# Optimization experiments

Hardware: AMD Instinct MI355X
Metric: run time of the kernel (lower is better)

Reference implementation:

```python
import jax, jax.numpy as jnp
import numpy as np

HEADS = 8
DIM_HEAD = 64
SCALE = DIM_HEAD ** -0.5


def setup_inputs() -> dict:
    key = jax.random.key(0)
    k1, k2, k3, k4 = jax.random.split(key, 4)
    dim = 512
    inner = HEADS * DIM_HEAD  # 512
    x = jax.random.normal(k1, (4, 2048, dim), dtype=jnp.float32)
    # torch nn.Linear weight layout: [out_features, in_features]
    w_qkv = jax.random.normal(k2, (inner * 3, dim), dtype=jnp.float32) * (dim ** -0.5)
    w_out = jax.random.normal(k3, (dim, inner), dtype=jnp.float32) * (inner ** -0.5)
    b_out = jax.random.normal(k4, (dim,), dtype=jnp.float32) * 0.01
    return {"x": x, "w_qkv": w_qkv, "w_out": w_out, "b_out": b_out}


def reference(x, w_qkv, w_out, b_out):
    b, n, _ = x.shape
    qkv = x @ w_qkv.T                                   # [b, n, 3*inner]
    q, k, v = jnp.split(qkv, 3, axis=-1)
    def to_heads(t):
        return t.reshape(b, n, HEADS, DIM_HEAD).transpose(0, 2, 1, 3)  # b h n d
    q, k, v = to_heads(q), to_heads(k), to_heads(v)
    dots = jnp.einsum('bhid,bhjd->bhij', q, k) * SCALE  # [b, h, n, n]
    attn = jax.nn.softmax(dots, axis=-1)
    out = jnp.einsum('bhij,bhjd->bhid', attn, v)        # [b, h, n, d]
    out = out.transpose(0, 2, 1, 3).reshape(b, n, HEADS * DIM_HEAD)
    return out @ w_out.T + b_out                        # [b, n, dim]
```

## Files before the change

kernel.cpp:

```cpp
#include <hip/hip_runtime.h>

typedef unsigned int u32;
typedef unsigned short u16;
typedef float f32x4 __attribute__((ext_vector_type(4)));
typedef u32 u32x4 __attribute__((ext_vector_type(4)));
typedef u32 u32x2 __attribute__((ext_vector_type(2)));

__device__ __forceinline__ u16 f2bf(float f) {
    u32 u = __builtin_bit_cast(u32, f);
    u = (u + 0x7FFFu + ((u >> 16) & 1u)) >> 16;
    return (u16)u;
}

__device__ __forceinline__ void mfma16(f32x4& d, const u32x4& a, const u32x4& b) {
    asm("v_mfma_f32_16x16x32_bf16 %0, %1, %2, %0" : "+v"(d) : "v"(a), "v"(b));
}

__device__ __forceinline__ float exp2a(float x) {
    float r;
    asm("v_exp_f32 %0, %1\n\ts_nop 1" : "=v"(r) : "v"(x));
    return r;
}
__device__ __forceinline__ u32 cvtpk(float lo, float hi) {
    u32 r;
    asm("v_cvt_pk_bf16_f32 %0, %1, %2" : "=v"(r) : "v"(lo), "v"(hi));
    return r;
}

__global__ __launch_bounds__(256) void cast_kernel(const float* __restrict__ in,
                                                   u16* __restrict__ out, int n) {
    int i = (blockIdx.x * 256 + threadIdx.x) * 8;
    if (i >= n) return;
    float4 a = *(const float4*)(in + i);
    float4 b = *(const float4*)(in + i + 4);
    u32x4 r;
    r.x = (u32)f2bf(a.x) | ((u32)f2bf(a.y) << 16);
    r.y = (u32)f2bf(a.z) | ((u32)f2bf(a.w) << 16);
    r.z = (u32)f2bf(b.x) | ((u32)f2bf(b.y) << 16);
    r.w = (u32)f2bf(b.z) | ((u32)f2bf(b.w) << 16);
    *(u32x4*)(out + i) = r;
}

template <int MODE>
__global__ __launch_bounds__(256) void gemm_bt(
    const u16* __restrict__ A, const u16* __restrict__ B, int K, int N,
    u16* __restrict__ qo, u16* __restrict__ ko, u16* __restrict__ vto,
    float* __restrict__ fo, const float* __restrict__ bias)
{
    __shared__ __align__(16) u16 Al[128][72];
    __shared__ __align__(16) u16 Bl[128][72];
    const int t = threadIdx.x;
    const int w = t >> 6, l = t & 63;
    const int wr = w >> 1, wc = w & 1;
    const int g = l >> 4, li = l & 15;
    const int m0 = blockIdx.x * 128, n0 = blockIdx.y * 128;

    const f32x4 z = {0.f, 0.f, 0.f, 0.f};
    f32x4 acc[4][4];
#pragma unroll
    for (int mi = 0; mi < 4; ++mi)
#pragma unroll
        for (int ni = 0; ni < 4; ++ni) acc[mi][ni] = z;

    const int srow = t >> 3, sch = (t & 7) * 8;
    for (int k0 = 0; k0 < K; k0 += 64) {
        __syncthreads();
#pragma unroll
        for (int rnd = 0; rnd < 4; ++rnd) {
            int row = srow + rnd * 32;
            u32x4 av = *(const u32x4*)(A + (size_t)(m0 + row) * K + k0 + sch);
            u32x4 bv = *(const u32x4*)(B + (size_t)(n0 + row) * K + k0 + sch);
            *(u32x4*)&Al[row][sch] = av;
            *(u32x4*)&Bl[row][sch] = bv;
        }
        __syncthreads();
#pragma unroll
        for (int ks = 0; ks < 2; ++ks) {
            u32x4 af[4], bf[4];
#pragma unroll
            for (int mi = 0; mi < 4; ++mi)
                af[mi] = *(const u32x4*)&Al[wr * 64 + mi * 16 + li][ks * 32 + g * 8];
#pragma unroll
            for (int ni = 0; ni < 4; ++ni)
                bf[ni] = *(const u32x4*)&Bl[wc * 64 + ni * 16 + li][ks * 32 + g * 8];
#pragma unroll
            for (int mi = 0; mi < 4; ++mi)
#pragma unroll
                for (int ni = 0; ni < 4; ++ni) mfma16(acc[mi][ni], af[mi], bf[ni]);
        }
    }

#pragma unroll
    for (int mi = 0; mi < 4; ++mi) {
#pragma unroll
        for (int ni = 0; ni < 4; ++ni) {
            int o = n0 + wc * 64 + ni * 16 + li;
            int m_base = m0 + wr * 64 + mi * 16 + g * 4;
            if (MODE == 0) {
                int part = o >> 9, oi = o & 511;
                int h = oi >> 6, d = oi & 63;
                int bb = m_base >> 11, nn = m_base & 2047;
                if (part == 2) {
                    u32x2 pv;
                    pv.x = (u32)f2bf(acc[mi][ni][0]) | ((u32)f2bf(acc[mi][ni][1]) << 16);
                    pv.y = (u32)f2bf(acc[mi][ni][2]) | ((u32)f2bf(acc[mi][ni][3]) << 16);
                    *(u32x2*)(vto + ((size_t)(bb * 8 + h) * 64 + d) * 2048 + nn) = pv;
                } else {
                    u16* dst = (part == 0) ? qo : ko;
#pragma unroll
                    for (int r = 0; r < 4; ++r)
                        dst[((size_t)(bb * 8 + h) * 2048 + nn + r) * 64 + d] =
                            f2bf(acc[mi][ni][r]);
                }
            } else {
#pragma unroll
                for (int r = 0; r < 4; ++r)
                    fo[(size_t)(m_base + r) * N + o] = acc[mi][ni][r] + bias[o];
            }
        }
    }
}

__global__ __launch_bounds__(256) void attn_kernel(
    const u16* __restrict__ Q, const u16* __restrict__ Kg,
    const u16* __restrict__ VT, u16* __restrict__ O)
{
    __shared__ __align__(16) u16 Kl[64 * 64];
    __shared__ __align__(16) u16 Vl[64 * 64];
    const int t = threadIdx.x;
    const int w = t >> 6, l = t & 63;
    const int g = l >> 4, li = l & 15;
    const int pair = blockIdx.y;
    const int q0 = blockIdx.x * 128 + w * 32;
    const float CEXP = 0.18033688011112042f;

    u32x4 qf[2][2];
#pragma unroll
    for (int qb = 0; qb < 2; ++qb)
#pragma unroll
        for (int f = 0; f < 2; ++f)
            qf[qb][f] = *(const u32x4*)(Q + ((size_t)pair * 2048 + q0 + qb * 16 + li) * 64
                                          + f * 32 + g * 8);

    const f32x4 z = {0.f, 0.f, 0.f, 0.f};
    f32x4 oacc[2][4];
#pragma unroll
    for (int qb = 0; qb < 2; ++qb)
#pragma unroll
        for (int dc = 0; dc < 4; ++dc) oacc[qb][dc] = z;
    float m_r[2] = {-1e30f, -1e30f};
    float l_r[2] = {0.f, 0.f};

    for (int kt = 0; kt < 32; ++kt) {
        __syncthreads();
#pragma unroll
        for (int i = 0; i < 2; ++i) {
            int s = i * 256 + t;
            int p = s >> 3, cp = s & 7;
            int cg = (cp ^ (p & 7)) * 8;
            int kr = (p & 0x23) | ((p & 0x0C) << 1) | ((p & 0x10) >> 2);
            u32x4 kv = *(const u32x4*)(Kg + ((size_t)pair * 2048 + kt * 64 + kr) * 64 + cg);
            u32x4 vv = *(const u32x4*)(VT + ((size_t)pair * 64 + p) * 2048 + kt * 64 + cg);
            *(u32x4*)&Kl[p * 64 + cp * 8] = kv;
            *(u32x4*)&Vl[p * 64 + cp * 8] = vv;
        }
        __syncthreads();

        f32x4 st[2][4];
#pragma unroll
        for (int qb = 0; qb < 2; ++qb)
#pragma unroll
            for (int kc = 0; kc < 4; ++kc) st[qb][kc] = z;
#pragma unroll
        for (int kc = 0; kc < 4; ++kc)
#pragma unroll
            for (int f = 0; f < 2; ++f) {
                u32x4 kf = *(const u32x4*)&Kl[(kc * 16 + li) * 64
                                              + (((4 * f + g) ^ (li & 7)) * 8)];
                mfma16(st[0][kc], kf, qf[0][f]);
                mfma16(st[1][kc], kf, qf[1][f]);
            }

        u32x4 pb[2][2];
#pragma unroll
        for (int qb = 0; qb < 2; ++qb) {
            float a0 = fmaxf(fmaxf(st[qb][0][0], st[qb][0][1]), fmaxf(st[qb][0][2], st[qb][0][3]));
            float a1 = fmaxf(fmaxf(st[qb][1][0], st[qb][1][1]), fmaxf(st[qb][1][2], st[qb][1][3]));
            float a2 = fmaxf(fmaxf(st[qb][2][0], st[qb][2][1]), fmaxf(st[qb][2][2], st[qb][2][3]));
            float a3 = fmaxf(fmaxf(st[qb][3][0], st[qb][3][1]), fmaxf(st[qb][3][2], st[qb][3][3]));
            float tmax = fmaxf(fmaxf(a0, a1), fmaxf(a2, a3)) * CEXP;
            if (__any(tmax - m_r[qb] > 8.0f)) {
                float m4 = tmax;
                m4 = fmaxf(m4, __shfl_xor(m4, 16));
                m4 = fmaxf(m4, __shfl_xor(m4, 32));
                float mn = fmaxf(m_r[qb], m4);
                float alpha = exp2a(m_r[qb] - mn);
                m_r[qb] = mn;
                l_r[qb] *= alpha;
#pragma unroll
                for (int dc = 0; dc < 4; ++dc) oacc[qb][dc] *= alpha;
            }
            float nm = -m_r[qb];
            float ls0 = 0.f, ls1 = 0.f;
#pragma unroll
            for (int kc = 0; kc < 4; ++kc) {
#pragma unroll
                for (int r = 0; r < 4; ++r) {
                    float pv = exp2a(__builtin_fmaf(st[qb][kc][r], CEXP, nm));
                    st[qb][kc][r] = pv;
                    if (r & 1) ls1 += pv; else ls0 += pv;
                }
            }
            l_r[qb] += ls0 + ls1;
#pragma unroll
            for (int f = 0; f < 2; ++f) {
                u32x4 pk;
                pk.x = cvtpk(st[qb][2 * f][0], st[qb][2 * f][1]);
                pk.y = cvtpk(st[qb][2 * f][2], st[qb][2 * f][3]);
                pk.z = cvtpk(st[qb][2 * f + 1][0], st[qb][2 * f + 1][1]);
                pk.w = cvtpk(st[qb][2 * f + 1][2], st[qb][2 * f + 1][3]);
                pb[qb][f] = pk;
            }
        }

#pragma unroll
        for (int dc = 0; dc < 4; ++dc)
#pragma unroll
            for (int f = 0; f < 2; ++f) {
                u32x4 vf = *(const u32x4*)&Vl[(dc * 16 + li) * 64
                                              + (((4 * f + g) ^ (li & 7)) * 8)];
                mfma16(oacc[0][dc], vf, pb[0][f]);
                mfma16(oacc[1][dc], vf, pb[1][f]);
            }
    }

    const int bb = pair >> 3, h = pair & 7;
#pragma unroll
    for (int qb = 0; qb < 2; ++qb) {
        float ls = l_r[qb];
        ls += __shfl_xor(ls, 16);
        ls += __shfl_xor(ls, 32);
        float inv = 1.f / ls;
        u16* orow = O + ((size_t)bb * 2048 + q0 + qb * 16 + li) * 512 + h * 64;
#pragma unroll
        for (int dc = 0; dc < 4; ++dc) {
            u32x2 pv;
            pv.x = cvtpk(oacc[qb][dc][0] * inv, oacc[qb][dc][1] * inv);
            pv.y = cvtpk(oacc[qb][dc][2] * inv, oacc[qb][dc][3] * inv);
            *(u32x2*)(orow + dc * 16 + 4 * g) = pv;
        }
    }
}

extern "C" void kernel_launch(void* const* d_in, const int* in_sizes, int n_in,
                              void* d_out, int out_size, void* d_ws, size_t ws_size,
                              hipStream_t stream) {
    const float* x     = (const float*)d_in[0];
    const float* w_qkv = (const float*)d_in[1];
    const float* w_out = (const float*)d_in[2];
    const float* b_out = (const float*)d_in[3];
    float* out = (float*)d_out;

    char* ws = (char*)d_ws;
    u16* xb = (u16*)(ws + 0);
    u16* o  = (u16*)(ws + 0);
    u16* wq = (u16*)(ws + 8388608);
    u16* wo = (u16*)(ws + 9961472);
    u16* q  = (u16*)(ws + 10485760);
    u16* kk = (u16*)(ws + 18874368);
    u16* vt = (u16*)(ws + 27262976);

    cast_kernel<<<2048, 256, 0, stream>>>(x, xb, 4194304);
    cast_kernel<<<384, 256, 0, stream>>>(w_qkv, wq, 786432);
    cast_kernel<<<128, 256, 0, stream>>>(w_out, wo, 262144);

    gemm_bt<0><<<dim3(64, 12), 256, 0, stream>>>(xb, wq, 512, 1536,
                                                 q, kk, vt, nullptr, nullptr);
    attn_kernel<<<dim3(16, 32), 256, 0, stream>>>(q, kk, vt, o);

    gemm_bt<1><<<dim3(64, 4), 256, 0, stream>>>(o, wo, 512, 512,
                                                nullptr, nullptr, nullptr, out, b_out);
}
```

Before: 109.1 us.

## Use 2 waves per attention block with 64 queries each; fold scale into Q

The attention kernel now runs 128 threads per block, with each wave owning 64 query rows instead of 32. This doubles the MFMA reuse of each K and V fragment read from LDS. The softmax scale times log2(e) is folded into Q during the QKV GEMM epilogue, which removes a multiply per score; the rescale threshold is adjusted to match. Exponentials are issued in batches of four and summed in a tree. The cost is higher register pressure, fewer waves per block for latency hiding, and rounding Q to bf16 after scaling.

Measured after the change: 137.5 us. 1.26x slower.

```diff
diff --git a/kernel.cpp b/kernel.cpp
--- a/kernel.cpp
+++ b/kernel.cpp
@@ -20,6 +20,14 @@
     float r;
     asm("v_exp_f32 %0, %1\n\ts_nop 1" : "=v"(r) : "v"(x));
     return r;
+}
+__device__ __forceinline__ void exp4(float& a, float& b, float& c, float& d) {
+    asm("v_exp_f32 %0, %0\n\t"
+        "v_exp_f32 %1, %1\n\t"
+        "v_exp_f32 %2, %2\n\t"
+        "v_exp_f32 %3, %3\n\t"
+        "s_nop 1"
+        : "+v"(a), "+v"(b), "+v"(c), "+v"(d));
 }
 __device__ __forceinline__ u32 cvtpk(float lo, float hi) {
     u32 r;
@@ -107,10 +115,11 @@
                     *(u32x2*)(vto + ((size_t)(bb * 8 + h) * 64 + d) * 2048 + nn) = pv;
                 } else {
                     u16* dst = (part == 0) ? qo : ko;
+                    const float sc = (part == 0) ? 0.18033688011112042f : 1.0f;
 #pragma unroll
                     for (int r = 0; r < 4; ++r)
                         dst[((size_t)(bb * 8 + h) * 2048 + nn + r) * 64 + d] =
-                            f2bf(acc[mi][ni][r]);
+                            f2bf(acc[mi][ni][r] * sc);
                 }
             } else {
 #pragma unroll
@@ -121,7 +130,7 @@
     }
 }
 
-__global__ __launch_bounds__(256) void attn_kernel(
+__global__ __launch_bounds__(128, 1) void attn_kernel(
     const u16* __restrict__ Q, const u16* __restrict__ Kg,
     const u16* __restrict__ VT, u16* __restrict__ O)
 {
@@ -131,44 +140,46 @@
     const int w = t >> 6, l = t & 63;
     const int g = l >> 4, li = l & 15;
     const int pair = blockIdx.y;
-    const int q0 = blockIdx.x * 128 + w * 32;
-    const float CEXP = 0.18033688011112042f;
-
-    u32x4 qf[2][2];
-#pragma unroll
-    for (int qb = 0; qb < 2; ++qb)
+    const int q0 = blockIdx.x * 128 + w * 64;
+
+    u32x4 qf[4][2];
+#pragma unroll
+    for (int qb = 0; qb < 4; ++qb)
 #pragma unroll
         for (int f = 0; f < 2; ++f)
             qf[qb][f] = *(const u32x4*)(Q + ((size_t)pair * 2048 + q0 + qb * 16 + li) * 64
                                           + f * 32 + g * 8);
 
     const f32x4 z = {0.f, 0.f, 0.f, 0.f};
-    f32x4 oacc[2][4];
-#pragma unroll
-    for (int qb = 0; qb < 2; ++qb)
+    f32x4 oacc[4][4];
+#pragma unroll
+    for (int qb = 0; qb < 4; ++qb)
 #pragma unroll
         for (int dc = 0; dc < 4; ++dc) oacc[qb][dc] = z;
-    float m_r[2] = {-1e30f, -1e30f};
-    float l_r[2] = {0.f, 0.f};
+    float m_r[4] = {-1e30f, -1e30f, -1e30f, -1e30f};
+    float l_r[4] = {0.f, 0.f, 0.f, 0.f};
+
+    const u16* kbase = Kg + (size_t)pair * 2048 * 64;
+    const u16* vbase = VT + (size_t)pair * 64 * 2048;
 
     for (int kt = 0; kt < 32; ++kt) {
         __syncthreads();
 #pragma unroll
-        for (int i = 0; i < 2; ++i) {
-            int s = i * 256 + t;
+        for (int i = 0; i < 4; ++i) {
+            int s = i * 128 + t;
             int p = s >> 3, cp = s & 7;
             int cg = (cp ^ (p & 7)) * 8;
             int kr = (p & 0x23) | ((p & 0x0C) << 1) | ((p & 0x10) >> 2);
-            u32x4 kv = *(const u32x4*)(Kg + ((size_t)pair * 2048 + kt * 64 + kr) * 64 + cg);
-            u32x4 vv = *(const u32x4*)(VT + ((size_t)pair * 64 + p) * 2048 + kt * 64 + cg);
-            *(u32x4*)&Kl[p * 64 + cp * 8] = kv;
-            *(u32x4*)&Vl[p * 64 + cp * 8] = vv;
-        }
-        __syncthreads();
-
-        f32x4 st[2][4];
-#pragma unroll
-        for (int qb = 0; qb < 2; ++qb)
+            *(u32x4*)&Kl[p * 64 + cp * 8] =
+                *(const u32x4*)(kbase + (size_t)kt * 4096 + kr * 64 + cg);
+            *(u32x4*)&Vl[p * 64 + cp * 8] =
+                *(const u32x4*)(vbase + (size_t)p * 2048 + kt * 64 + cg);
+        }
+        __syncthreads();
+
+        f32x4 st[4][4];
+#pragma unroll
+        for (int qb = 0; qb < 4; ++qb)
 #pragma unroll
             for (int kc = 0; kc < 4; ++kc) st[qb][kc] = z;
 #pragma unroll
@@ -177,19 +188,19 @@
             for (int f = 0; f < 2; ++f) {
                 u32x4 kf = *(const u32x4*)&Kl[(kc * 16 + li) * 64
                                               + (((4 * f + g) ^ (li & 7)) * 8)];
-                mfma16(st[0][kc], kf, qf[0][f]);
-                mfma16(st[1][kc], kf, qf[1][f]);
-            }
-
-        u32x4 pb[2][2];
-#pragma unroll
-        for (int qb = 0; qb < 2; ++qb) {
+#pragma unroll
+                for (int qb = 0; qb < 4; ++qb) mfma16(st[qb][kc], kf, qf[qb][f]);
+            }
+
+        u32x4 pb[4][2];
+#pragma unroll
+        for (int qb = 0; qb < 4; ++qb) {
             float a0 = fmaxf(fmaxf(st[qb][0][0], st[qb][0][1]), fmaxf(st[qb][0][2], st[qb][0][3]));
             float a1 = fmaxf(fmaxf(st[qb][1][0], st[qb][1][1]), fmaxf(st[qb][1][2], st[qb][1][3]));
             float a2 = fmaxf(fmaxf(st[qb][2][0], st[qb][2][1]), fmaxf(st[qb][2][2], st[qb][2][3]));
             float a3 = fmaxf(fmaxf(st[qb][3][0], st[qb][3][1]), fmaxf(st[qb][3][2], st[qb][3][3]));
-            float tmax = fmaxf(fmaxf(a0, a1), fmaxf(a2, a3)) * CEXP;
-            if (__any(tmax - m_r[qb] > 8.0f)) {
+            float tmax = fmaxf(fmaxf(a0, a1), fmaxf(a2, a3));
+            if (__any(tmax - m_r[qb] > 11.0f)) {
                 float m4 = tmax;
                 m4 = fmaxf(m4, __shfl_xor(m4, 16));
                 m4 = fmaxf(m4, __shfl_xor(m4, 32));
@@ -201,24 +212,28 @@
                 for (int dc = 0; dc < 4; ++dc) oacc[qb][dc] *= alpha;
             }
             float nm = -m_r[qb];
-            float ls0 = 0.f, ls1 = 0.f;
+            float pv[16];
 #pragma unroll
             for (int kc = 0; kc < 4; ++kc) {
 #pragma unroll
-                for (int r = 0; r < 4; ++r) {
-                    float pv = exp2a(__builtin_fmaf(st[qb][kc][r], CEXP, nm));
-                    st[qb][kc][r] = pv;
-                    if (r & 1) ls1 += pv; else ls0 += pv;
-                }
-            }
-            l_r[qb] += ls0 + ls1;
+                for (int r = 0; r < 4; ++r) pv[kc * 4 + r] = st[qb][kc][r] + nm;
+            }
+            exp4(pv[0], pv[1], pv[2], pv[3]);
+            exp4(pv[4], pv[5], pv[6], pv[7]);
+            exp4(pv[8], pv[9], pv[10], pv[11]);
+            exp4(pv[12], pv[13], pv[14], pv[15]);
+            float s0 = (pv[0] + pv[1]) + (pv[2] + pv[3]);
+            float s1 = (pv[4] + pv[5]) + (pv[6] + pv[7]);
+            float s2 = (pv[8] + pv[9]) + (pv[10] + pv[11]);
+            float s3 = (pv[12] + pv[13]) + (pv[14] + pv[15]);
+            l_r[qb] += (s0 + s1) + (s2 + s3);
 #pragma unroll
             for (int f = 0; f < 2; ++f) {
                 u32x4 pk;
-                pk.x = cvtpk(st[qb][2 * f][0], st[qb][2 * f][1]);
-                pk.y = cvtpk(st[qb][2 * f][2], st[qb][2 * f][3]);
-                pk.z = cvtpk(st[qb][2 * f + 1][0], st[qb][2 * f + 1][1]);
-                pk.w = cvtpk(st[qb][2 * f + 1][2], st[qb][2 * f + 1][3]);
+                pk.x = cvtpk(pv[8 * f + 0], pv[8 * f + 1]);
+                pk.y = cvtpk(pv[8 * f + 2], pv[8 * f + 3]);
+                pk.z = cvtpk(pv[8 * f + 4], pv[8 * f + 5]);
+                pk.w = cvtpk(pv[8 * f + 6], pv[8 * f + 7]);
                 pb[qb][f] = pk;
             }
         }
@@ -229,14 +244,14 @@
             for (int f = 0; f < 2; ++f) {
                 u32x4 vf = *(const u32x4*)&Vl[(dc * 16 + li) * 64
                                               + (((4 * f + g) ^ (li & 7)) * 8)];
-                mfma16(oacc[0][dc], vf, pb[0][f]);
-                mfma16(oacc[1][dc], vf, pb[1][f]);
+#pragma unroll
+                for (int qb = 0; qb < 4; ++qb) mfma16(oacc[qb][dc], vf, pb[qb][f]);
             }
     }
 
     const int bb = pair >> 3, h = pair & 7;
 #pragma unroll
-    for (int qb = 0; qb < 2; ++qb) {
+    for (int qb = 0; qb < 4; ++qb) {
         float ls = l_r[qb];
         ls += __shfl_xor(ls, 16);
         ls += __shfl_xor(ls, 32);
@@ -276,7 +291,7 @@
 
     gemm_bt<0><<<dim3(64, 12), 256, 0, stream>>>(xb, wq, 512, 1536,
                                                  q, kk, vt, nullptr, nullptr);
-    attn_kernel<<<dim3(16, 32), 256, 0, stream>>>(q, kk, vt, o);
+    attn_kernel<<<dim3(16, 32), 128, 0, stream>>>(q, kk, vt, o);
 
     gemm_bt<1><<<dim3(64, 4), 256, 0, stream>>>(o, wo, 512, 512,
                                                 nullptr, nullptr, nullptr, out, b_out);
```
